# Optimization experiments

Measured on AMD Instinct MI355X. Metric: run time of the kernel, lower is better.

Reference implementation:

```python
import jax, jax.numpy as jnp
import numpy as np

N = 4096        # mentions
H = 768         # hidden size
MAXK = 64       # max candidates per mention
TOTAL = N * 32  # total ragged candidate pairs (avg k = 32)
FAISS_WEIGHT = 0.5


def _ragged_indices():
    rng = np.random.default_rng(0)
    d = rng.integers(-31, 32, size=N // 2)
    lengths = np.concatenate([32 + d, 32 - d]).astype(np.int64)  # sum == TOTAL, each in [1, 64]
    mention_idx = np.repeat(np.arange(N, dtype=np.int32), lengths)
    offsets = np.concatenate([[0], np.cumsum(lengths)[:-1]])
    col_idx = (np.arange(TOTAL) - np.repeat(offsets, lengths)).astype(np.int32)
    return mention_idx, col_idx


def setup_inputs() -> dict:
    key = jax.random.key(0)
    ks = jax.random.split(key, 6)
    mention_idx, col_idx = _ragged_indices()
    return {
        "mention_embs": jax.random.normal(ks[0], (N, H), dtype=jnp.float32),
        "candidate_embs": jax.random.normal(ks[1], (TOTAL, H), dtype=jnp.float32),
        "W1": jax.random.normal(ks[2], (2 * H, H), dtype=jnp.float32) * 0.02,
        "b1": jnp.zeros((H,), dtype=jnp.float32),
        "W2": jax.random.normal(ks[3], (H, 1), dtype=jnp.float32) * 0.02,
        "b2": jnp.zeros((1,), dtype=jnp.float32),
        "faiss_prior": jax.random.uniform(ks[4], (N, MAXK), dtype=jnp.float32),
        "nota_bias": jnp.zeros((), dtype=jnp.float32),
        "mention_idx": jnp.asarray(mention_idx),
        "col_idx": jnp.asarray(col_idx),
    }


def reference(mention_embs, candidate_embs, W1, b1, W2, b2, faiss_prior, nota_bias, mention_idx, col_idx):
    n, max_k = faiss_prior.shape
    # gather mention embedding per ragged pair, concat with candidate embedding
    x = jnp.concatenate([mention_embs[mention_idx], candidate_embs], axis=1)  # [T, 2H]
    h = jax.nn.relu(x @ W1 + b1)                                              # [T, H]
    pair_scores = (h @ W2 + b2)[:, 0]                                         # [T]
    # scatter ragged scores into padded [N, MAXK] (padding stays 0)
    scores = jnp.zeros((n, max_k), dtype=pair_scores.dtype).at[mention_idx, col_idx].set(pair_scores)
    scores = scores + FAISS_WEIGHT * faiss_prior  # torch adds prior to all first k_use cols
    nota_col = jnp.broadcast_to(nota_bias.reshape(1, 1), (n, 1))
    return jnp.concatenate([scores, nota_col], axis=1)  # [N, MAXK+1]
```

## Files before the change

### kernel.cpp

```cpp
#include <hip/hip_runtime.h>

typedef float floatx4 __attribute__((ext_vector_type(4)));
typedef short short8 __attribute__((ext_vector_type(8)));

#define H 768
#define NMENT 4096
#define TOTALP 131072
#define MAXK 64
#define BM 256
#define BN 256
#define BK 64
#define LDA_S 72

__device__ __forceinline__ unsigned short f32_to_bf16(float f) {
    unsigned int u = __builtin_bit_cast(unsigned int, f);
    u = u + 0x7FFFu + ((u >> 16) & 1u);
    return (unsigned short)(u >> 16);
}

__device__ __forceinline__ short8 pack8(float4 a, float4 b) {
    short8 r;
    r[0] = (short)f32_to_bf16(a.x); r[1] = (short)f32_to_bf16(a.y);
    r[2] = (short)f32_to_bf16(a.z); r[3] = (short)f32_to_bf16(a.w);
    r[4] = (short)f32_to_bf16(b.x); r[5] = (short)f32_to_bf16(b.y);
    r[6] = (short)f32_to_bf16(b.z); r[7] = (short)f32_to_bf16(b.w);
    return r;
}

__device__ __forceinline__ void glds16(const unsigned short* g, unsigned short* l) {
    __builtin_amdgcn_global_load_lds(
        (const __attribute__((address_space(1))) unsigned int*)g,
        (__attribute__((address_space(3))) unsigned int*)l, 16, 0, 0);
}

__global__ void k0_transpose(const float* __restrict__ W1,
                             unsigned short* __restrict__ BtA,
                             unsigned short* __restrict__ BtB) {
    __shared__ float tile[32][33];
    const int k0 = blockIdx.x * 32;
    const int n0 = blockIdx.y * 32;
    const int tx = threadIdx.x;
    const int ty = threadIdx.y;
#pragma unroll
    for (int i = 0; i < 4; ++i)
        tile[ty + i * 8][tx] = W1[(k0 + ty + i * 8) * H + n0 + tx];
    __syncthreads();
    unsigned short* dst = (k0 < H) ? BtA : BtB;
    const int kb = (k0 >= H) ? (k0 - H) : k0;
#pragma unroll
    for (int i = 0; i < 4; ++i) {
        const int n = n0 + ty + i * 8;
        dst[n * H + kb + tx] = f32_to_bf16(tile[tx][ty + i * 8]);
    }
}

__global__ void k3_init_out(const float* __restrict__ faiss,
                            const float* __restrict__ nota,
                            float* __restrict__ out) {
    const int i = blockIdx.x * 256 + threadIdx.x;
    if (i < NMENT * (MAXK + 1)) {
        const int n = i / (MAXK + 1);
        const int j = i - n * (MAXK + 1);
        out[i] = (j < MAXK) ? 0.5f * faiss[n * MAXK + j] : nota[0];
    }
}

template<int MODE>
__global__ __launch_bounds__(1024, 4)
void gemm_core(const float* __restrict__ A, const unsigned short* __restrict__ Bt,
               const float* __restrict__ M, const float* __restrict__ W2,
               const float* __restrict__ b2, const int* __restrict__ mention_idx,
               const int* __restrict__ col_idx, const float* __restrict__ b1,
               float* __restrict__ outp) {
    __shared__ unsigned short ldsA[BM * LDA_S];
    __shared__ unsigned short ldsB[BN * BK];
    __shared__ float w2s[BN];
    __shared__ float scoreBuf[BM * 4];

    const int bid = blockIdx.x;
    int t_tile, nsplit;
    if (MODE == 1) {
        const int g = bid / 24, rr = bid % 24;
        t_tile = g * 8 + (rr & 7);
        nsplit = rr >> 3;
    } else {
        t_tile = bid % 16;
        nsplit = bid / 16;
    }
    const int t0 = t_tile * BM;
    const int n0 = nsplit * BN;

    const int tid = threadIdx.x;
    const int lane = tid & 63;
    const int w = tid >> 6;
    const int wm = w >> 2, wn = w & 3;
    const int l15 = lane & 15, quad = lane >> 4;

    if (tid < BN) w2s[tid] = (MODE == 1) ? W2[n0 + tid] : b1[n0 + tid];

    floatx4 acc[4][4];
#pragma unroll
    for (int mi = 0; mi < 4; ++mi)
#pragma unroll
        for (int ni = 0; ni < 4; ++ni)
            acc[mi][ni] = floatx4{0.f, 0.f, 0.f, 0.f};

    const int arow = tid >> 2;
    const int aseg = tid & 3;
    const float* agp = A + (size_t)(t0 + arow) * H + aseg * 16;
    unsigned short* alp = &ldsA[arow * LDA_S + aseg * 16];

    for (int kc = 0; kc < H; kc += BK) {
        float4 v0 = *(const float4*)(agp + kc);
        float4 v1 = *(const float4*)(agp + kc + 4);
        float4 v2 = *(const float4*)(agp + kc + 8);
        float4 v3 = *(const float4*)(agp + kc + 12);
        *(short8*)(alp) = pack8(v0, v1);
        *(short8*)(alp + 8) = pack8(v2, v3);
#pragma unroll
        for (int i = 0; i < 2; ++i) {
            const int br = w * 16 + i * 8;
            const int r = br + (lane >> 3);
            const int cd = (lane & 7) ^ (r & 7);
            glds16(Bt + (size_t)(n0 + r) * H + kc + cd * 8, &ldsB[br * BK]);
        }
        __syncthreads();
#pragma unroll
        for (int ks = 0; ks < 2; ++ks) {
            short8 a[4], b[4];
#pragma unroll
            for (int mi = 0; mi < 4; ++mi)
                a[mi] = *(const short8*)&ldsA[(wm * 64 + mi * 16 + l15) * LDA_S + ks * 32 + quad * 8];
#pragma unroll
            for (int ni = 0; ni < 4; ++ni) {
                const int nr = wn * 64 + ni * 16 + l15;
                const int slot = (quad + ks * 4) ^ (nr & 7);
                b[ni] = *(const short8*)&ldsB[nr * BK + slot * 8];
            }
#pragma unroll
            for (int mi = 0; mi < 4; ++mi)
#pragma unroll
                for (int ni = 0; ni < 4; ++ni)
                    acc[mi][ni] = __builtin_amdgcn_mfma_f32_16x16x32_bf16(a[mi], b[ni], acc[mi][ni], 0, 0, 0);
        }
        __syncthreads();
    }

    if (MODE == 0) {
#pragma unroll
        for (int ni = 0; ni < 4; ++ni) {
            const int nl = wn * 64 + ni * 16 + l15;
            const float bv = w2s[nl];
#pragma unroll
            for (int mi = 0; mi < 4; ++mi)
#pragma unroll
                for (int r = 0; r < 4; ++r) {
                    const int row = t0 + wm * 64 + mi * 16 + quad * 4 + r;
                    outp[(size_t)row * H + n0 + nl] = acc[mi][ni][r] + bv;
                }
        }
    } else {
#pragma unroll
        for (int mi = 0; mi < 4; ++mi) {
#pragma unroll
            for (int r = 0; r < 4; ++r) {
                const int rl = wm * 64 + mi * 16 + quad * 4 + r;
                const int m = mention_idx[t0 + rl];
                const float* Mrow = M + (size_t)m * H + n0;
                float s = 0.f;
#pragma unroll
                for (int ni = 0; ni < 4; ++ni) {
                    const int nl = wn * 64 + ni * 16 + l15;
                    const float v = acc[mi][ni][r] + Mrow[nl];
                    s = fmaf(fmaxf(v, 0.f), w2s[nl], s);
                }
                s += __shfl_xor(s, 1, 64);
                s += __shfl_xor(s, 2, 64);
                s += __shfl_xor(s, 4, 64);
                s += __shfl_xor(s, 8, 64);
                if (l15 == 0) scoreBuf[rl * 4 + wn] = s;
            }
        }
        __syncthreads();
        if (tid < BM) {
            const int t = t0 + tid;
            float tot = scoreBuf[tid * 4] + scoreBuf[tid * 4 + 1] +
                        scoreBuf[tid * 4 + 2] + scoreBuf[tid * 4 + 3];
            if (nsplit == 0) tot += b2[0];
            atomicAdd(&outp[(size_t)mention_idx[t] * (MAXK + 1) + col_idx[t]], tot);
        }
    }
}

extern "C" void kernel_launch(void* const* d_in, const int* in_sizes, int n_in,
                              void* d_out, int out_size, void* d_ws, size_t ws_size,
                              hipStream_t stream) {
    const float* ment  = (const float*)d_in[0];
    const float* cand  = (const float*)d_in[1];
    const float* W1    = (const float*)d_in[2];
    const float* b1    = (const float*)d_in[3];
    const float* W2    = (const float*)d_in[4];
    const float* b2    = (const float*)d_in[5];
    const float* faiss = (const float*)d_in[6];
    const float* nota  = (const float*)d_in[7];
    const int* mention_idx = (const int*)d_in[8];
    const int* col_idx = (const int*)d_in[9];
    float* out = (float*)d_out;

    unsigned short* BtA = (unsigned short*)d_ws;
    unsigned short* BtB = BtA + H * H;
    float* M = (float*)(BtB + H * H);

    k0_transpose<<<dim3(48, 24), dim3(32, 8), 0, stream>>>(W1, BtA, BtB);
    k3_init_out<<<(NMENT * (MAXK + 1) + 255) / 256, 256, 0, stream>>>(faiss, nota, out);
    gemm_core<0><<<48, 1024, 0, stream>>>(ment, BtA, nullptr, nullptr, nullptr,
                                          nullptr, nullptr, b1, M);
    gemm_core<1><<<1536, 1024, 0, stream>>>(cand, BtB, M, W2, b2,
                                            mention_idx, col_idx, nullptr, out);
}
```

Measured before the change: 783.4 us.

## Double-buffer LDS tiles in GEMM to overlap global loads with MFMA compute

Doubles the A and B LDS buffers so the next K-slice is loaded (B via global_load_lds, A via registers then packed to bf16) while MFMAs run on the current slice. This removes one of the two barriers per K iteration and hides global-load latency within a block. LDS per block roughly doubles, to about 144KB, which likely cuts resident blocks per CU from two to one and reduces latency hiding across blocks.

```diff
diff --git a/kernel.cpp b/kernel.cpp
--- a/kernel.cpp
+++ b/kernel.cpp
@@ -72,8 +72,8 @@
                const float* __restrict__ b2, const int* __restrict__ mention_idx,
                const int* __restrict__ col_idx, const float* __restrict__ b1,
                float* __restrict__ outp) {
-    __shared__ unsigned short ldsA[BM * LDA_S];
-    __shared__ unsigned short ldsB[BN * BK];
+    __shared__ unsigned short ldsA[2 * BM * LDA_S];
+    __shared__ unsigned short ldsB[2 * BN * BK];
     __shared__ float w2s[BN];
     __shared__ float scoreBuf[BM * 4];
 
@@ -108,43 +108,72 @@
     const int arow = tid >> 2;
     const int aseg = tid & 3;
     const float* agp = A + (size_t)(t0 + arow) * H + aseg * 16;
-    unsigned short* alp = &ldsA[arow * LDA_S + aseg * 16];
-
-    for (int kc = 0; kc < H; kc += BK) {
+    const int aoff = arow * LDA_S + aseg * 16;
+
+#define COMPUTE_TILE(CUR)                                                                 \
+    do {                                                                                  \
+        const unsigned short* lA = ldsA + (CUR) * (BM * LDA_S);                           \
+        const unsigned short* lB = ldsB + (CUR) * (BN * BK);                              \
+        _Pragma("unroll")                                                                 \
+        for (int ks = 0; ks < 2; ++ks) {                                                  \
+            short8 a[4], b[4];                                                            \
+            _Pragma("unroll")                                                             \
+            for (int mi = 0; mi < 4; ++mi)                                                \
+                a[mi] = *(const short8*)&lA[(wm * 64 + mi * 16 + l15) * LDA_S + ks * 32 + quad * 8]; \
+            _Pragma("unroll")                                                             \
+            for (int ni = 0; ni < 4; ++ni) {                                              \
+                const int nr = wn * 64 + ni * 16 + l15;                                   \
+                const int slot = (quad + ks * 4) ^ (nr & 7);                              \
+                b[ni] = *(const short8*)&lB[nr * BK + slot * 8];                          \
+            }                                                                             \
+            _Pragma("unroll")                                                             \
+            for (int mi = 0; mi < 4; ++mi)                                                \
+                _Pragma("unroll")                                                         \
+                for (int ni = 0; ni < 4; ++ni)                                            \
+                    acc[mi][ni] = __builtin_amdgcn_mfma_f32_16x16x32_bf16(a[mi], b[ni], acc[mi][ni], 0, 0, 0); \
+        }                                                                                 \
+    } while (0)
+
+    {
+        float4 v0 = *(const float4*)(agp);
+        float4 v1 = *(const float4*)(agp + 4);
+        float4 v2 = *(const float4*)(agp + 8);
+        float4 v3 = *(const float4*)(agp + 12);
+#pragma unroll
+        for (int i = 0; i < 2; ++i) {
+            const int br = w * 16 + i * 8;
+            const int r = br + (lane >> 3);
+            const int cd = (lane & 7) ^ (r & 7);
+            glds16(Bt + (size_t)(n0 + r) * H + cd * 8, &ldsB[br * BK]);
+        }
+        *(short8*)(&ldsA[aoff]) = pack8(v0, v1);
+        *(short8*)(&ldsA[aoff + 8]) = pack8(v2, v3);
+        __syncthreads();
+    }
+
+    int cur = 0;
+    for (int kc = BK; kc < H; kc += BK) {
         float4 v0 = *(const float4*)(agp + kc);
         float4 v1 = *(const float4*)(agp + kc + 4);
         float4 v2 = *(const float4*)(agp + kc + 8);
         float4 v3 = *(const float4*)(agp + kc + 12);
-        *(short8*)(alp) = pack8(v0, v1);
-        *(short8*)(alp + 8) = pack8(v2, v3);
+        unsigned short* lbn = ldsB + (cur ^ 1) * (BN * BK);
 #pragma unroll
         for (int i = 0; i < 2; ++i) {
             const int br = w * 16 + i * 8;
             const int r = br + (lane >> 3);
             const int cd = (lane & 7) ^ (r & 7);
-            glds16(Bt + (size_t)(n0 + r) * H + kc + cd * 8, &ldsB[br * BK]);
-        }
+            glds16(Bt + (size_t)(n0 + r) * H + kc + cd * 8, lbn + br * BK);
+        }
+        COMPUTE_TILE(cur);
+        unsigned short* lan = ldsA + (cur ^ 1) * (BM * LDA_S);
+        *(short8*)(&lan[aoff]) = pack8(v0, v1);
+        *(short8*)(&lan[aoff + 8]) = pack8(v2, v3);
         __syncthreads();
-#pragma unroll
-        for (int ks = 0; ks < 2; ++ks) {
-            short8 a[4], b[4];
-#pragma unroll
-            for (int mi = 0; mi < 4; ++mi)
-                a[mi] = *(const short8*)&ldsA[(wm * 64 + mi * 16 + l15) * LDA_S + ks * 32 + quad * 8];
-#pragma unroll
-            for (int ni = 0; ni < 4; ++ni) {
-                const int nr = wn * 64 + ni * 16 + l15;
-                const int slot = (quad + ks * 4) ^ (nr & 7);
-                b[ni] = *(const short8*)&ldsB[nr * BK + slot * 8];
-            }
-#pragma unroll
-            for (int mi = 0; mi < 4; ++mi)
-#pragma unroll
-                for (int ni = 0; ni < 4; ++ni)
-                    acc[mi][ni] = __builtin_amdgcn_mfma_f32_16x16x32_bf16(a[mi], b[ni], acc[mi][ni], 0, 0, 0);
-        }
-        __syncthreads();
-    }
+        cur ^= 1;
+    }
+    COMPUTE_TILE(cur);
+#undef COMPUTE_TILE
 
     if (MODE == 0) {
 #pragma unroll
```

New measurement: 723.2 us. 7.7% less time.

## Double-buffer LDS and enlarge per-wave tile with interleaved prefetch in GEMM

Applied to the files above, without the earlier changes.

Switches the GEMM to 512-thread blocks where each wave computes a 128x64 tile, and double-buffers the A and B LDS tiles so loads for the next k-step are issued while MFMAs run on the current one. Compute is split into four phases with barriers and raised wave priority around the MFMA clusters. The score reduction buffer now reuses A's LDS space. This is meant to hide global/LDS load latency and raise MFMA density, at the cost of higher register and LDS use, likely limiting occupancy to one block per CU.

```diff
diff --git a/kernel.cpp b/kernel.cpp
--- a/kernel.cpp
+++ b/kernel.cpp
@@ -11,6 +11,9 @@
 #define BN 256
 #define BK 64
 #define LDA_S 72
+#define ASZ (BM * LDA_S)
+#define BSZ (BN * BK)
+#define NKT (H / BK)
 
 __device__ __forceinline__ unsigned short f32_to_bf16(float f) {
     unsigned int u = __builtin_bit_cast(unsigned int, f);
@@ -66,16 +69,15 @@
 }
 
 template<int MODE>
-__global__ __launch_bounds__(1024, 4)
+__global__ __launch_bounds__(512, 2)
 void gemm_core(const float* __restrict__ A, const unsigned short* __restrict__ Bt,
                const float* __restrict__ M, const float* __restrict__ W2,
                const float* __restrict__ b2, const int* __restrict__ mention_idx,
                const int* __restrict__ col_idx, const float* __restrict__ b1,
                float* __restrict__ outp) {
-    __shared__ unsigned short ldsA[BM * LDA_S];
-    __shared__ unsigned short ldsB[BN * BK];
+    __shared__ unsigned short ldsA[2 * ASZ];
+    __shared__ unsigned short ldsB[2 * BSZ];
     __shared__ float w2s[BN];
-    __shared__ float scoreBuf[BM * 4];
 
     const int bid = blockIdx.x;
     int t_tile, nsplit;
@@ -98,80 +100,156 @@
 
     if (tid < BN) w2s[tid] = (MODE == 1) ? W2[n0 + tid] : b1[n0 + tid];
 
-    floatx4 acc[4][4];
-#pragma unroll
-    for (int mi = 0; mi < 4; ++mi)
+    floatx4 acc[8][4];
+#pragma unroll
+    for (int mf = 0; mf < 8; ++mf)
 #pragma unroll
         for (int ni = 0; ni < 4; ++ni)
-            acc[mi][ni] = floatx4{0.f, 0.f, 0.f, 0.f};
-
-    const int arow = tid >> 2;
-    const int aseg = tid & 3;
-    const float* agp = A + (size_t)(t0 + arow) * H + aseg * 16;
-    unsigned short* alp = &ldsA[arow * LDA_S + aseg * 16];
-
-    for (int kc = 0; kc < H; kc += BK) {
-        float4 v0 = *(const float4*)(agp + kc);
-        float4 v1 = *(const float4*)(agp + kc + 4);
-        float4 v2 = *(const float4*)(agp + kc + 8);
-        float4 v3 = *(const float4*)(agp + kc + 12);
-        *(short8*)(alp) = pack8(v0, v1);
-        *(short8*)(alp + 8) = pack8(v2, v3);
-#pragma unroll
-        for (int i = 0; i < 2; ++i) {
-            const int br = w * 16 + i * 8;
-            const int r = br + (lane >> 3);
-            const int cd = (lane & 7) ^ (r & 7);
-            glds16(Bt + (size_t)(n0 + r) * H + kc + cd * 8, &ldsB[br * BK]);
-        }
+            acc[mf][ni] = floatx4{0.f, 0.f, 0.f, 0.f};
+
+    const int arow = tid >> 1;
+    const int aseg = tid & 1;
+    const float* agp = A + (size_t)(t0 + arow) * H + aseg * 32;
+    const int aoff = arow * LDA_S + aseg * 32;
+
+    short8 a[4], b[4];
+
+#define READ_A(LA, MH, KS)                                                                \
+    _Pragma("unroll")                                                                     \
+    for (int mi = 0; mi < 4; ++mi)                                                        \
+        a[mi] = *(const short8*)&(LA)[(wm * 128 + ((MH) * 4 + mi) * 16 + l15) * LDA_S + (KS) * 32 + quad * 8];
+
+#define READ_B(LB, KS)                                                                    \
+    _Pragma("unroll")                                                                     \
+    for (int ni = 0; ni < 4; ++ni) {                                                      \
+        const int nr = wn * 64 + ni * 16 + l15;                                           \
+        const int slot = (quad + (KS) * 4) ^ (nr & 7);                                    \
+        b[ni] = *(const short8*)&(LB)[nr * BK + slot * 8];                                \
+    }
+
+#define MFMA16(MH)                                                                        \
+    _Pragma("unroll")                                                                     \
+    for (int mi = 0; mi < 4; ++mi)                                                        \
+        _Pragma("unroll")                                                                 \
+        for (int ni = 0; ni < 4; ++ni)                                                    \
+            acc[(MH) * 4 + mi][ni] =                                                      \
+                __builtin_amdgcn_mfma_f32_16x16x32_bf16(a[mi], b[ni], acc[(MH) * 4 + mi][ni], 0, 0, 0);
+
+#define ALIGN_PIN()                                                                       \
+    __builtin_amdgcn_s_barrier();                                                         \
+    asm volatile("s_waitcnt lgkmcnt(0)");                                                 \
+    __builtin_amdgcn_sched_barrier(0);
+
+#define STAGE_B(SB, KC)                                                                   \
+    _Pragma("unroll")                                                                     \
+    for (int i = 0; i < 4; ++i) {                                                         \
+        const int br = w * 32 + i * 8;                         \
+        const int r = br + (lane >> 3);                                                   \
+        const int cd = (lane & 7) ^ (r & 7);     \
+        glds16(Bt + (size_t)(n0 + r) * H + (KC) + cd * 8, (SB) + br * BK);                \
+    }
+
+    {
+        const float4 v0 = *(const float4*)(agp);      const float4 v1 = *(const float4*)(agp + 4);
+        const float4 v2 = *(const float4*)(agp + 8);  const float4 v3 = *(const float4*)(agp + 12);
+        const float4 v4 = *(const float4*)(agp + 16); const float4 v5 = *(const float4*)(agp + 20);
+        const float4 v6 = *(const float4*)(agp + 24); const float4 v7 = *(const float4*)(agp + 28);
+        STAGE_B(ldsB, 0);
+        *(short8*)(&ldsA[aoff])      = pack8(v0, v1);
+        *(short8*)(&ldsA[aoff + 8])  = pack8(v2, v3);
+        *(short8*)(&ldsA[aoff + 16]) = pack8(v4, v5);
+        *(short8*)(&ldsA[aoff + 24]) = pack8(v6, v7);
         __syncthreads();
-#pragma unroll
-        for (int ks = 0; ks < 2; ++ks) {
-            short8 a[4], b[4];
-#pragma unroll
-            for (int mi = 0; mi < 4; ++mi)
-                a[mi] = *(const short8*)&ldsA[(wm * 64 + mi * 16 + l15) * LDA_S + ks * 32 + quad * 8];
+    }
+
+    int cur = 0;
+    for (int t = 0; t < NKT; ++t) {
+        const unsigned short* lA = ldsA + cur * ASZ;
+        const unsigned short* lB = ldsB + cur * BSZ;
+        unsigned short* sA = ldsA + (cur ^ 1) * ASZ;
+        unsigned short* sB = ldsB + (cur ^ 1) * BSZ;
+        const int kn = (t + 1) * BK;
+        const bool stage = (t < NKT - 1);
+        float4 v0, v1, v2, v3, v4, v5, v6, v7;
+
+        if (stage) {
+            v0 = *(const float4*)(agp + kn);      v1 = *(const float4*)(agp + kn + 4);
+            v2 = *(const float4*)(agp + kn + 8);  v3 = *(const float4*)(agp + kn + 12);
+            v4 = *(const float4*)(agp + kn + 16); v5 = *(const float4*)(agp + kn + 20);
+            v6 = *(const float4*)(agp + kn + 24); v7 = *(const float4*)(agp + kn + 28);
+        }
+        READ_B(lB, 0);
+        READ_A(lA, 0, 0);
+        ALIGN_PIN();
+        __builtin_amdgcn_s_setprio(1);
+        MFMA16(0);
+        __builtin_amdgcn_s_setprio(0);
+        __builtin_amdgcn_s_barrier();
+
+        if (stage) { STAGE_B(sB, kn); }
+        READ_A(lA, 1, 0);
+        ALIGN_PIN();
+        __builtin_amdgcn_s_setprio(1);
+        MFMA16(1);
+        __builtin_amdgcn_s_setprio(0);
+        __builtin_amdgcn_s_barrier();
+
+        READ_B(lB, 1);
+        READ_A(lA, 0, 1);
+        ALIGN_PIN();
+        __builtin_amdgcn_s_setprio(1);
+        MFMA16(0);
+        __builtin_amdgcn_s_setprio(0);
+        __builtin_amdgcn_s_barrier();
+
+        if (stage) {
+            *(short8*)(&sA[aoff])      = pack8(v0, v1);
+            *(short8*)(&sA[aoff + 8])  = pack8(v2, v3);
+            *(short8*)(&sA[aoff + 16]) = pack8(v4, v5);
+            *(short8*)(&sA[aoff + 24]) = pack8(v6, v7);
+        }
+        READ_A(lA, 1, 1);
+        ALIGN_PIN();
+        __builtin_amdgcn_s_setprio(1);
+        MFMA16(1);
+        __builtin_amdgcn_s_setprio(0);
+        __syncthreads();
+        cur ^= 1;
+    }
+
+#undef READ_A
+#undef READ_B
+#undef MFMA16
+#undef ALIGN_PIN
+#undef STAGE_B
+
+    if (MODE == 0) {
+#pragma unroll
+        for (int mf = 0; mf < 8; ++mf)
 #pragma unroll
             for (int ni = 0; ni < 4; ++ni) {
-                const int nr = wn * 64 + ni * 16 + l15;
-                const int slot = (quad + ks * 4) ^ (nr & 7);
-                b[ni] = *(const short8*)&ldsB[nr * BK + slot * 8];
+                const int nl = wn * 64 + ni * 16 + l15;
+                const float bv = w2s[nl];
+#pragma unroll
+                for (int r = 0; r < 4; ++r) {
+                    const int row = t0 + wm * 128 + mf * 16 + quad * 4 + r;
+                    outp[(size_t)row * H + n0 + nl] = acc[mf][ni][r] + bv;
+                }
             }
-#pragma unroll
-            for (int mi = 0; mi < 4; ++mi)
-#pragma unroll
-                for (int ni = 0; ni < 4; ++ni)
-                    acc[mi][ni] = __builtin_amdgcn_mfma_f32_16x16x32_bf16(a[mi], b[ni], acc[mi][ni], 0, 0, 0);
-        }
-        __syncthreads();
-    }
-
-    if (MODE == 0) {
-#pragma unroll
-        for (int ni = 0; ni < 4; ++ni) {
-            const int nl = wn * 64 + ni * 16 + l15;
-            const float bv = w2s[nl];
-#pragma unroll
-            for (int mi = 0; mi < 4; ++mi)
-#pragma unroll
-                for (int r = 0; r < 4; ++r) {
-                    const int row = t0 + wm * 64 + mi * 16 + quad * 4 + r;
-                    outp[(size_t)row * H + n0 + nl] = acc[mi][ni][r] + bv;
-                }
-        }
     } else {
-#pragma unroll
-        for (int mi = 0; mi < 4; ++mi) {
+        float* scoreBuf = (float*)ldsA;
+#pragma unroll
+        for (int mf = 0; mf < 8; ++mf) {
 #pragma unroll
             for (int r = 0; r < 4; ++r) {
-                const int rl = wm * 64 + mi * 16 + quad * 4 + r;
+                const int rl = wm * 128 + mf * 16 + quad * 4 + r;
                 const int m = mention_idx[t0 + rl];
                 const float* Mrow = M + (size_t)m * H + n0;
                 float s = 0.f;
 #pragma unroll
                 for (int ni = 0; ni < 4; ++ni) {
                     const int nl = wn * 64 + ni * 16 + l15;
-                    const float v = acc[mi][ni][r] + Mrow[nl];
+                    const float v = acc[mf][ni][r] + Mrow[nl];
                     s = fmaf(fmaxf(v, 0.f), w2s[nl], s);
                 }
                 s += __shfl_xor(s, 1, 64);
@@ -213,8 +291,8 @@
 
     k0_transpose<<<dim3(48, 24), dim3(32, 8), 0, stream>>>(W1, BtA, BtB);
     k3_init_out<<<(NMENT * (MAXK + 1) + 255) / 256, 256, 0, stream>>>(faiss, nota, out);
-    gemm_core<0><<<48, 1024, 0, stream>>>(ment, BtA, nullptr, nullptr, nullptr,
-                                          nullptr, nullptr, b1, M);
-    gemm_core<1><<<1536, 1024, 0, stream>>>(cand, BtB, M, W2, b2,
-                                            mention_idx, col_idx, nullptr, out);
-}
+    gemm_core<0><<<48, 512, 0, stream>>>(ment, BtA, nullptr, nullptr, nullptr,
+                                         nullptr, nullptr, b1, M);
+    gemm_core<1><<<1536, 512, 0, stream>>>(cand, BtB, M, W2, b2,
+                                           mention_idx, col_idx, nullptr, out);
+}
```

Result: slower. 868.0 us (+10.8%).
